# Optimization experiments

Hardware: AMD Instinct MI355X
Metric: run time of the kernel (lower is better)

The kernel has to match this reference:

```python
import jax, jax.numpy as jnp
import numpy as np

G, P, F, K = 256, 512, 4, 6   # graphs, nodes/graph, features, knn k
N = G * P

def _prelu(x, a):
    return jnp.where(x >= 0, x, a * x)

def _knn_edges(x):
    # per-graph brute-force kNN (k=6, no self loops), flow source->target
    xg = x.reshape(G, P, F)
    sq = jnp.sum(xg * xg, -1)                                   # [G,P]
    d = sq[:, :, None] + sq[:, None, :] - 2.0 * jnp.einsum('gpf,gqf->gpq', xg, xg)
    d = d + jnp.eye(P, dtype=x.dtype) * 1e10                    # exclude self
    _, idx = jax.lax.top_k(-d, K)                               # [G,P,K] neighbors
    off = (jnp.arange(G) * P)[:, None, None]
    src = (idx + off).reshape(-1)                               # message sources
    tgt = jnp.broadcast_to(jnp.arange(N).reshape(G, P, 1), (G, P, K)).reshape(-1)
    return src, tgt

def setup_inputs():
    key = jax.random.key(0)
    ks = jax.random.split(key, 8)
    f = lambda k, s: jax.random.normal(k, s, jnp.float32) * 0.1
    return {
        "x": jax.random.normal(ks[0], (N, F), jnp.float32),
        "batch": jnp.arange(N, dtype=jnp.int32) // P,
        "pre_W1": f(ks[1], (F, F)), "pre_b1": jnp.zeros((F,), jnp.float32),
        "pre_a1": jnp.full((F,), 0.25, jnp.float32),
        "pre_W2": f(ks[2], (F, F)), "pre_b2": jnp.zeros((F,), jnp.float32),
        "pre_a2": jnp.full((F,), 0.25, jnp.float32),
        "bn_g": jnp.ones((F,), jnp.float32), "bn_b": jnp.zeros((F,), jnp.float32),
        "act_a": jnp.full((F,), 0.25, jnp.float32),
        "conv_Wm": f(ks[3], (4, F, F)), "conv_bm": jnp.zeros((4, F), jnp.float32),
        "hlv_W1": f(ks[4], (5 * F, 5 * F)), "hlv_b1": jnp.zeros((5 * F,), jnp.float32),
        "hlv_W2": f(ks[5], (5 * F, 1)), "hlv_b2": jnp.zeros((1,), jnp.float32),
    }

def reference(x, batch, pre_W1, pre_b1, pre_a1, pre_W2, pre_b2, pre_a2,
              bn_g, bn_b, act_a, conv_Wm, conv_bm, hlv_W1, hlv_b1, hlv_W2, hlv_b2):
    src, tgt = _knn_edges(x)                                    # knn on raw x
    # pre_nn: Linear-PReLU-Linear-PReLU-BatchNorm (batch stats, training mode)
    h = _prelu(x @ pre_W1 + pre_b1, pre_a1)
    h = _prelu(h @ pre_W2 + pre_b2, pre_a2)
    mu = jnp.mean(h, 0)
    var = jnp.var(h, 0)
    h = (h - mu) / jnp.sqrt(var + 1e-5) * bn_g + bn_b
    xs = [h]
    for i in range(4):
        # GeneralConv (PyG defaults): sum-aggregate lin_msg(x_j) + identity skip
        msg = h[src] @ conv_Wm[i] + conv_bm[i]                  # [E,F]
        aggr = jax.ops.segment_sum(msg, tgt, num_segments=N)    # [N,F]
        h = _prelu(aggr + h, act_a)                             # shared PReLU act
        xs.append(h)
    hc = jnp.concatenate(xs, axis=-1)                           # JK 'cat' -> [N,5F]
    pooled = jax.ops.segment_sum(hc, batch, num_segments=G)     # global_add_pool
    out = jax.nn.relu(pooled @ hlv_W1 + hlv_b1) @ hlv_W2 + hlv_b2
    return out
```

## Files before the change

### kernel.cpp

```cpp
#include <hip/hip_runtime.h>

#define GG 256
#define PP 512
#define FF 4
#define KK 6
#define NN (GG*PP)

__device__ __forceinline__ unsigned umin_(unsigned a, unsigned b){ return a<b?a:b; }
__device__ __forceinline__ unsigned umax_(unsigned a, unsigned b){ return a>b?a:b; }
__device__ __forceinline__ float finf(){ return __int_as_float(0x7f800000); }

__device__ __forceinline__ unsigned mmap32(float d){
    int bb = __float_as_int(d);
    int t = bb >> 31;
    return (unsigned)(bb ^ (t | (int)0x80000000));
}

__device__ __forceinline__ void cas6_u64(uint64_t (&B)[6], uint64_t kv)
{
    bool c1 = kv < B[1]; bool c2 = kv < B[2]; bool c3 = kv < B[3];
    bool c4 = kv < B[4]; bool c5 = kv < B[5];
    B[0] = c1 ? B[1] : kv;
    B[1] = c2 ? B[2] : (c1 ? kv : B[1]);
    B[2] = c3 ? B[3] : (c2 ? kv : B[2]);
    B[3] = c4 ? B[4] : (c3 ? kv : B[3]);
    B[4] = c5 ? B[5] : (c4 ? kv : B[4]);
    B[5] = c5 ? kv : B[5];
}

#define INS7U(v){                                  \
    unsigned n0=umin_(M0,(v));                     \
    unsigned n1=umin_(M1,umax_((v),M0));           \
    unsigned n2=umin_(M2,umax_((v),M1));           \
    unsigned n3=umin_(M3,umax_((v),M2));           \
    unsigned n4=umin_(M4,umax_((v),M3));           \
    unsigned n5=umin_(M5,umax_((v),M4));           \
    unsigned n6=umin_(M6,umax_((v),M5));           \
    M0=n0;M1=n1;M2=n2;M3=n3;M4=n4;M5=n5;M6=n6; }

__global__ __launch_bounds__(512) void scan_kernel(
    const float* __restrict__ x,
    const float* __restrict__ pre_W1, const float* __restrict__ pre_b1, const float* __restrict__ pre_a1,
    const float* __restrict__ pre_W2, const float* __restrict__ pre_b2, const float* __restrict__ pre_a2,
    float* __restrict__ bn_part,
    int* __restrict__ knn_idx)
{
    __shared__ float4   xm2s[PP];
    __shared__ float    sqs[PP];
    __shared__ ushort   gmp16[32][PP];
    __shared__ float    Tv[PP];
    __shared__ unsigned mbuf[16][PP];
    __shared__ float    wred[8][8];

    const int t = threadIdx.x;
    const int g = blockIdx.x;
    const int gbase = g * PP;
    const int w = t >> 6, lane = t & 63;
    const int wu = __builtin_amdgcn_readfirstlane(w);
    const int qb = wu * 64;

    float4 xt = ((const float4*)x)[gbase + t];
    xm2s[t] = make_float4(-2.0f*xt.x, -2.0f*xt.y, -2.0f*xt.z, -2.0f*xt.w);
    sqs[t]  = xt.x*xt.x + xt.y*xt.y + xt.z*xt.z + xt.w*xt.w;
    {
        float h1[FF], h2[FF];
#pragma unroll
        for (int fo=0;fo<FF;fo++){
            float m = xt.x*pre_W1[0*FF+fo] + xt.y*pre_W1[1*FF+fo]
                    + xt.z*pre_W1[2*FF+fo] + xt.w*pre_W1[3*FF+fo] + pre_b1[fo];
            h1[fo] = m >= 0.0f ? m : pre_a1[fo]*m;
        }
#pragma unroll
        for (int fo=0;fo<FF;fo++){
            float m = h1[0]*pre_W2[0*FF+fo] + h1[1]*pre_W2[1*FF+fo]
                    + h1[2]*pre_W2[2*FF+fo] + h1[3]*pre_W2[3*FF+fo] + pre_b2[fo];
            h2[fo] = m >= 0.0f ? m : pre_a2[fo]*m;
        }
        float v[8];
#pragma unroll
        for (int f=0;f<4;f++){ v[f]=h2[f]; v[4+f]=h2[f]*h2[f]; }
#pragma unroll
        for (int off=32; off; off>>=1){
#pragma unroll
            for (int f=0;f<8;f++) v[f] += __shfl_down(v[f], off);
        }
        if (lane==0){
#pragma unroll
            for (int f=0;f<8;f++) wred[w][f]=v[f];
        }
    }
    __syncthreads();
    if (t < 8){
        float a=0;
#pragma unroll
        for (int w2=0;w2<8;w2++) a += wred[w2][t];
        bn_part[t*GG + g] = a;
    }

    float4 xp[8];
#pragma unroll
    for (int j=0;j<8;j++){
        float4 v = xm2s[lane + 64*j];
        xp[j] = make_float4(-0.5f*v.x, -0.5f*v.y, -0.5f*v.z, -0.5f*v.w);
    }
    const float INF = finf();

#pragma unroll 1
    for (int grp=0; grp<4; grp++){
        float gm[8];
#pragma unroll
        for (int j=0;j<8;j++) gm[j]=INF;
#pragma unroll
        for (int i2=0;i2<8;i2++){
            const int q0 = qb + grp*16 + i2*2;
            float4 a = xm2s[q0], b = xm2s[q0+1];
            float2 sq = *(const float2*)&sqs[q0];
#pragma unroll
            for (int j=0;j<8;j++){
                float da = fmaf(a.x,xp[j].x, fmaf(a.y,xp[j].y, fmaf(a.z,xp[j].z, fmaf(a.w,xp[j].w, sq.x))));
                float db = fmaf(b.x,xp[j].x, fmaf(b.y,xp[j].y, fmaf(b.z,xp[j].z, fmaf(b.w,xp[j].w, sq.y))));
                gm[j] = fminf(gm[j], fminf(da, db));
            }
        }
#pragma unroll
        for (int j=0;j<8;j++){
            unsigned u = mmap32(gm[j]);
            unsigned r = (u >> 16) + ((u & 0xFFFFu) ? 1u : 0u);
            r = umin_(r, 0xFFFFu);
            gmp16[wu*4 + grp][lane + 64*j] = (ushort)r;
        }
    }
    __syncthreads();

    {
        unsigned M0=~0u,M1=~0u,M2=~0u,M3=~0u,M4=~0u,M5=~0u,M6=~0u;
#pragma unroll
        for (int r=0;r<32;r++){
            unsigned v = gmp16[r][t];
            INS7U(v);
        }
        unsigned Tc = M6 << 16;
        Tv[t] = (Tc & 0x80000000u) ? __uint_as_float(Tc ^ 0x80000000u)
                                   : __uint_as_float(~Tc);
    }
    __syncthreads();

    float Tf[8];
#pragma unroll
    for (int j=0;j<8;j++) Tf[j] = Tv[lane + 64*j];

#pragma unroll 1
    for (int h=0; h<2; h++){
        unsigned m[8];
#pragma unroll
        for (int j=0;j<8;j++) m[j]=0;
#pragma unroll 4
        for (int i2=0;i2<16;i2++){
            const int q0 = qb + h*32 + i2*2;
            float4 a = xm2s[q0], b = xm2s[q0+1];
            float2 sq = *(const float2*)&sqs[q0];
#pragma unroll
            for (int j=0;j<8;j++){
                float da = fmaf(a.x,xp[j].x, fmaf(a.y,xp[j].y, fmaf(a.z,xp[j].z, fmaf(a.w,xp[j].w, sq.x))));
                float db = fmaf(b.x,xp[j].x, fmaf(b.y,xp[j].y, fmaf(b.z,xp[j].z, fmaf(b.w,xp[j].w, sq.y))));
                m[j] = m[j] + m[j] + (da <= Tf[j] ? 1u : 0u);
                m[j] = m[j] + m[j] + (db <= Tf[j] ? 1u : 0u);
            }
        }
#pragma unroll
        for (int j=0;j<8;j++) mbuf[wu*2 + h][lane + 64*j] = m[j];
    }
    __syncthreads();

    {
        float4 xmq = xm2s[t];
        float4 xq = make_float4(-0.5f*xmq.x, -0.5f*xmq.y, -0.5f*xmq.z, -0.5f*xmq.w);
        uint64_t B[6];
#pragma unroll
        for (int j2=0;j2<6;j2++) B[j2] = ~0ull;
#pragma unroll 1
        for (int r=0;r<16;r++){
            unsigned m = mbuf[r][t];
            const int base = (r>>1)*64 + (r&1)*32;
            while (m){
                int c = __builtin_clz(m);
                m &= ~(0x80000000u >> c);
                int idx = base + c;
                float4 a = xm2s[idx];
                float d = fmaf(a.x,xq.x, fmaf(a.y,xq.y, fmaf(a.z,xq.z, fmaf(a.w,xq.w, sqs[idx]))));
                uint64_t key = ((uint64_t)mmap32(d) << 32) | (unsigned)idx;
                if (idx == t) key = ~0ull;
                if (key < B[0]) cas6_u64(B, key);
            }
        }
#pragma unroll
        for (int j2=0;j2<6;j2++)
            knn_idx[j2*NN + gbase + t] = (int)(B[j2] & 0xFFFFFFFFull);
    }
}

__global__ __launch_bounds__(512) void graph_kernel(
    const float* __restrict__ x,
    const int* __restrict__ knn_idx,
    const float* __restrict__ bn_part,
    const float* __restrict__ pre_W1, const float* __restrict__ pre_b1, const float* __restrict__ pre_a1,
    const float* __restrict__ pre_W2, const float* __restrict__ pre_b2, const float* __restrict__ pre_a2,
    const float* __restrict__ bn_g, const float* __restrict__ bn_b,
    const float* __restrict__ act_a,
    const float* __restrict__ conv_Wm, const float* __restrict__ conv_bm,
    const float* __restrict__ hlv_W1, const float* __restrict__ hlv_b1,
    const float* __restrict__ hlv_W2, const float* __restrict__ hlv_b2,
    float* __restrict__ out)
{
    __shared__ float4 hbuf[PP];
    __shared__ float wred[8][4];
    __shared__ float pooled[20];
    __shared__ float stats[8];
    __shared__ float hid[20];
    const int g = blockIdx.x, p = threadIdx.x;
    const int gp = g*PP + p;

    if (p < 64){
        int vv = p>>3, j = p&7;
        float acc = 0.0f;
        for (int i=j;i<GG;i+=8) acc += bn_part[vv*GG + i];
        acc += __shfl_xor(acc,1); acc += __shfl_xor(acc,2); acc += __shfl_xor(acc,4);
        if (j==0) stats[vv] = acc;
    }
    __syncthreads();
    if (p < 4){
        float mu  = stats[p]   * (1.0f/NN);
        float var = stats[4+p] * (1.0f/NN) - mu*mu;
        stats[p]   = mu;
        stats[4+p] = 1.0f / sqrtf(var + 1e-5f);
    }

    float4 xt = ((const float4*)x)[gp];
    float h1[FF], h2[FF];
#pragma unroll
    for (int fo=0;fo<FF;fo++){
        float m = xt.x*pre_W1[0*FF+fo] + xt.y*pre_W1[1*FF+fo]
                + xt.z*pre_W1[2*FF+fo] + xt.w*pre_W1[3*FF+fo] + pre_b1[fo];
        h1[fo] = m >= 0.0f ? m : pre_a1[fo]*m;
    }
#pragma unroll
    for (int fo=0;fo<FF;fo++){
        float m = h1[0]*pre_W2[0*FF+fo] + h1[1]*pre_W2[1*FF+fo]
                + h1[2]*pre_W2[2*FF+fo] + h1[3]*pre_W2[3*FF+fo] + pre_b2[fo];
        h2[fo] = m >= 0.0f ? m : pre_a2[fo]*m;
    }
    __syncthreads();

    float hp[4];
#pragma unroll
    for (int f=0;f<4;f++)
        hp[f] = (h2[f] - stats[f]) * stats[4+f] * bn_g[f] + bn_b[f];
    hbuf[p] = make_float4(hp[0],hp[1],hp[2],hp[3]);
    int nb[KK];
#pragma unroll
    for (int j=0;j<KK;j++) nb[j] = knn_idx[j*NN + gp];

    auto block_accum = [&](const float* h, int slice){
        float v0=h[0], v1=h[1], v2=h[2], v3=h[3];
#pragma unroll
        for (int off=32; off; off>>=1){
            v0 += __shfl_down(v0,off); v1 += __shfl_down(v1,off);
            v2 += __shfl_down(v2,off); v3 += __shfl_down(v3,off);
        }
        int w = p>>6;
        if ((p&63)==0){ wred[w][0]=v0; wred[w][1]=v1; wred[w][2]=v2; wred[w][3]=v3; }
        __syncthreads();
        if (p < 4){
            float a=0;
#pragma unroll
            for (int w2=0;w2<8;w2++) a += wred[w2][p];
            pooled[slice*4+p] = a;
        }
        __syncthreads();
    };

    block_accum(hp, 0);

#pragma unroll 1
    for (int L=0; L<4; L++){
        float4 sm = make_float4(0.f,0.f,0.f,0.f);
#pragma unroll
        for (int j=0;j<KK;j++){
            float4 hn = hbuf[nb[j]];
            sm.x+=hn.x; sm.y+=hn.y; sm.z+=hn.z; sm.w+=hn.w;
        }
        const float* W  = conv_Wm + L*16;
        const float* bm = conv_bm + L*4;
        float nh[4];
#pragma unroll
        for (int fo=0;fo<4;fo++){
            float m = sm.x*W[0*4+fo] + sm.y*W[1*4+fo] + sm.z*W[2*4+fo] + sm.w*W[3*4+fo]
                    + 6.0f*bm[fo] + hp[fo];
            float a = act_a[fo];
            nh[fo] = m >= 0.0f ? m : a*m;
        }
        __syncthreads();
        hbuf[p] = make_float4(nh[0],nh[1],nh[2],nh[3]);
#pragma unroll
        for (int f=0;f<4;f++) hp[f]=nh[f];
        block_accum(hp, L+1);
    }

    if (p < 20){
        float acc = hlv_b1[p];
#pragma unroll 1
        for (int k2=0;k2<20;k2++) acc += pooled[k2]*hlv_W1[k2*20+p];
        hid[p] = acc > 0.0f ? acc : 0.0f;
    }
    __syncthreads();
    if (p == 0){
        float o = hlv_b2[0];
#pragma unroll 1
        for (int j=0;j<20;j++) o += hid[j]*hlv_W2[j];
        out[g] = o;
    }
}

extern "C" void kernel_launch(void* const* d_in, const int* in_sizes, int n_in,
                              void* d_out, int out_size, void* d_ws, size_t ws_size,
                              hipStream_t stream)
{
    const float* x      = (const float*)d_in[0];
    const float* pre_W1 = (const float*)d_in[2];
    const float* pre_b1 = (const float*)d_in[3];
    const float* pre_a1 = (const float*)d_in[4];
    const float* pre_W2 = (const float*)d_in[5];
    const float* pre_b2 = (const float*)d_in[6];
    const float* pre_a2 = (const float*)d_in[7];
    const float* bn_g   = (const float*)d_in[8];
    const float* bn_b   = (const float*)d_in[9];
    const float* act_a  = (const float*)d_in[10];
    const float* conv_Wm= (const float*)d_in[11];
    const float* conv_bm= (const float*)d_in[12];
    const float* hlv_W1 = (const float*)d_in[13];
    const float* hlv_b1 = (const float*)d_in[14];
    const float* hlv_W2 = (const float*)d_in[15];
    const float* hlv_b2 = (const float*)d_in[16];

    char* ws = (char*)d_ws;
    int*   knn     = (int*)ws;
    float* bn_part = (float*)(ws + (size_t)6*NN*sizeof(int));

    scan_kernel<<<GG, PP, 0, stream>>>(x, pre_W1,pre_b1,pre_a1,
                                       pre_W2,pre_b2,pre_a2, bn_part, knn);
    graph_kernel<<<GG, PP, 0, stream>>>(x, knn, bn_part,
                                        pre_W1,pre_b1,pre_a1, pre_W2,pre_b2,pre_a2,
                                        bn_g,bn_b, act_a, conv_Wm,conv_bm,
                                        hlv_W1,hlv_b1,hlv_W2,hlv_b2,
                                        (float*)d_out);
}
```

Before: 57.08 us.

## Split kNN scan across two blocks per graph, halving query rows per block

The scan kernel now launches two blocks per graph, and each block handles half of the 512 query points. This halves per-thread register arrays and shrinks the shared scratch buffers, which are aliased into one, to allow more resident blocks per CU. In exchange, both blocks redundantly load the graph's points, and only half the threads do the final threshold and top-k selection stages. A launch_bounds occupancy hint is also added.

```diff
diff --git a/kernel.cpp b/kernel.cpp
--- a/kernel.cpp
+++ b/kernel.cpp
@@ -38,7 +38,7 @@
     unsigned n6=umin_(M6,umax_((v),M5));           \
     M0=n0;M1=n1;M2=n2;M3=n3;M4=n4;M5=n5;M6=n6; }
 
-__global__ __launch_bounds__(512) void scan_kernel(
+__global__ __launch_bounds__(512, 4) void scan_kernel(
     const float* __restrict__ x,
     const float* __restrict__ pre_W1, const float* __restrict__ pre_b1, const float* __restrict__ pre_a1,
     const float* __restrict__ pre_W2, const float* __restrict__ pre_b2, const float* __restrict__ pre_a2,
@@ -47,13 +47,17 @@
 {
     __shared__ float4   xm2s[PP];
     __shared__ float    sqs[PP];
-    __shared__ ushort   gmp16[32][PP];
-    __shared__ float    Tv[PP];
-    __shared__ unsigned mbuf[16][PP];
+    __shared__ unsigned ubuf[16*256];
+    __shared__ float    Tv[256];
     __shared__ float    wred[8][8];
 
+    ushort   (*gmp16)[256] = (ushort  (*)[256])ubuf;
+    unsigned (*mbuf)[256]  = (unsigned(*)[256])ubuf;
+
     const int t = threadIdx.x;
-    const int g = blockIdx.x;
+    const int bid = blockIdx.x;
+    const int g = bid >> 1, half = bid & 1;
+    const int tbase = half * 256;
     const int gbase = g * PP;
     const int w = t >> 6, lane = t & 63;
     const int wu = __builtin_amdgcn_readfirstlane(w);
@@ -62,7 +66,7 @@
     float4 xt = ((const float4*)x)[gbase + t];
     xm2s[t] = make_float4(-2.0f*xt.x, -2.0f*xt.y, -2.0f*xt.z, -2.0f*xt.w);
     sqs[t]  = xt.x*xt.x + xt.y*xt.y + xt.z*xt.z + xt.w*xt.w;
-    {
+    if (half == 0){
         float h1[FF], h2[FF];
 #pragma unroll
         for (int fo=0;fo<FF;fo++){
@@ -90,40 +94,40 @@
         }
     }
     __syncthreads();
-    if (t < 8){
+    if (half == 0 && t < 8){
         float a=0;
 #pragma unroll
         for (int w2=0;w2<8;w2++) a += wred[w2][t];
         bn_part[t*GG + g] = a;
     }
 
-    float4 xp[8];
-#pragma unroll
-    for (int j=0;j<8;j++){
-        float4 v = xm2s[lane + 64*j];
+    float4 xp[4];
+#pragma unroll
+    for (int j=0;j<4;j++){
+        float4 v = xm2s[tbase + lane + 64*j];
         xp[j] = make_float4(-0.5f*v.x, -0.5f*v.y, -0.5f*v.z, -0.5f*v.w);
     }
     const float INF = finf();
 
 #pragma unroll 1
     for (int grp=0; grp<4; grp++){
-        float gm[8];
-#pragma unroll
-        for (int j=0;j<8;j++) gm[j]=INF;
+        float gm[4];
+#pragma unroll
+        for (int j=0;j<4;j++) gm[j]=INF;
 #pragma unroll
         for (int i2=0;i2<8;i2++){
             const int q0 = qb + grp*16 + i2*2;
             float4 a = xm2s[q0], b = xm2s[q0+1];
             float2 sq = *(const float2*)&sqs[q0];
 #pragma unroll
-            for (int j=0;j<8;j++){
+            for (int j=0;j<4;j++){
                 float da = fmaf(a.x,xp[j].x, fmaf(a.y,xp[j].y, fmaf(a.z,xp[j].z, fmaf(a.w,xp[j].w, sq.x))));
                 float db = fmaf(b.x,xp[j].x, fmaf(b.y,xp[j].y, fmaf(b.z,xp[j].z, fmaf(b.w,xp[j].w, sq.y))));
                 gm[j] = fminf(gm[j], fminf(da, db));
             }
         }
 #pragma unroll
-        for (int j=0;j<8;j++){
+        for (int j=0;j<4;j++){
             unsigned u = mmap32(gm[j]);
             unsigned r = (u >> 16) + ((u & 0xFFFFu) ? 1u : 0u);
             r = umin_(r, 0xFFFFu);
@@ -132,7 +136,7 @@
     }
     __syncthreads();
 
-    {
+    if (t < 256){
         unsigned M0=~0u,M1=~0u,M2=~0u,M3=~0u,M4=~0u,M5=~0u,M6=~0u;
 #pragma unroll
         for (int r=0;r<32;r++){
@@ -145,22 +149,22 @@
     }
     __syncthreads();
 
-    float Tf[8];
-#pragma unroll
-    for (int j=0;j<8;j++) Tf[j] = Tv[lane + 64*j];
+    float Tf[4];
+#pragma unroll
+    for (int j=0;j<4;j++) Tf[j] = Tv[lane + 64*j];
 
 #pragma unroll 1
     for (int h=0; h<2; h++){
-        unsigned m[8];
-#pragma unroll
-        for (int j=0;j<8;j++) m[j]=0;
+        unsigned m[4];
+#pragma unroll
+        for (int j=0;j<4;j++) m[j]=0;
 #pragma unroll 4
         for (int i2=0;i2<16;i2++){
             const int q0 = qb + h*32 + i2*2;
             float4 a = xm2s[q0], b = xm2s[q0+1];
             float2 sq = *(const float2*)&sqs[q0];
 #pragma unroll
-            for (int j=0;j<8;j++){
+            for (int j=0;j<4;j++){
                 float da = fmaf(a.x,xp[j].x, fmaf(a.y,xp[j].y, fmaf(a.z,xp[j].z, fmaf(a.w,xp[j].w, sq.x))));
                 float db = fmaf(b.x,xp[j].x, fmaf(b.y,xp[j].y, fmaf(b.z,xp[j].z, fmaf(b.w,xp[j].w, sq.y))));
                 m[j] = m[j] + m[j] + (da <= Tf[j] ? 1u : 0u);
@@ -168,12 +172,13 @@
             }
         }
 #pragma unroll
-        for (int j=0;j<8;j++) mbuf[wu*2 + h][lane + 64*j] = m[j];
-    }
-    __syncthreads();
-
-    {
-        float4 xmq = xm2s[t];
+        for (int j=0;j<4;j++) mbuf[wu*2 + h][lane + 64*j] = m[j];
+    }
+    __syncthreads();
+
+    if (t < 256){
+        const int pt = tbase + t;
+        float4 xmq = xm2s[pt];
         float4 xq = make_float4(-0.5f*xmq.x, -0.5f*xmq.y, -0.5f*xmq.z, -0.5f*xmq.w);
         uint64_t B[6];
 #pragma unroll
@@ -189,13 +194,13 @@
                 float4 a = xm2s[idx];
                 float d = fmaf(a.x,xq.x, fmaf(a.y,xq.y, fmaf(a.z,xq.z, fmaf(a.w,xq.w, sqs[idx]))));
                 uint64_t key = ((uint64_t)mmap32(d) << 32) | (unsigned)idx;
-                if (idx == t) key = ~0ull;
+                if (idx == pt) key = ~0ull;
                 if (key < B[0]) cas6_u64(B, key);
             }
         }
 #pragma unroll
         for (int j2=0;j2<6;j2++)
-            knn_idx[j2*NN + gbase + t] = (int)(B[j2] & 0xFFFFFFFFull);
+            knn_idx[j2*NN + gbase + pt] = (int)(B[j2] & 0xFFFFFFFFull);
     }
 }
 
@@ -346,8 +351,8 @@
     int*   knn     = (int*)ws;
     float* bn_part = (float*)(ws + (size_t)6*NN*sizeof(int));
 
-    scan_kernel<<<GG, PP, 0, stream>>>(x, pre_W1,pre_b1,pre_a1,
-                                       pre_W2,pre_b2,pre_a2, bn_part, knn);
+    scan_kernel<<<GG*2, PP, 0, stream>>>(x, pre_W1,pre_b1,pre_a1,
+                                         pre_W2,pre_b2,pre_a2, bn_part, knn);
     graph_kernel<<<GG, PP, 0, stream>>>(x, knn, bn_part,
                                         pre_W1,pre_b1,pre_a1, pre_W2,pre_b2,pre_a2,
                                         bn_g,bn_b, act_a, conv_Wm,conv_bm,
```

After: 58.80 us. 1.03x slower.
